# Performance work log

Measured on AMD Instinct MI355X. Metric: run time of the kernel, lower is better.

The kernel has to match this reference:

```python
import jax, jax.numpy as jnp
import numpy as np

B, S, E, H = 2, 2048, 1024, 16
D = E // H  # head_dim = 64
EPS = 1e-6


def _angle_decay():
    # angle: 1/10000**linspace(0,1,D//2), each value repeated twice (interleaved)
    a = 1.0 / (10000.0 ** jnp.linspace(0.0, 1.0, D // 2))
    angle = jnp.repeat(a, 2)  # [D]
    decay = jnp.log(1.0 - 2.0 ** (-5.0 - jnp.arange(H, dtype=jnp.float32)))  # [H]
    return angle, decay


def _rel_pos(slen):
    angle, decay = _angle_decay()
    idx = jnp.arange(slen, dtype=jnp.float32)
    sin = jnp.sin(idx[:, None] * angle[None, :])  # [S, D]
    cos = jnp.cos(idx[:, None] * angle[None, :])  # [S, D]
    diff = idx[:, None] - idx[None, :]            # [S, S]
    tril = diff >= 0
    masked = jnp.where(tril, diff, jnp.inf)
    mask = jnp.exp(masked * decay[:, None, None])  # [H, S, S]; exp(-inf)=0 on upper tri
    mask = jnp.nan_to_num(mask)
    mask = mask / jnp.sqrt(jnp.sum(mask, axis=-1, keepdims=True))
    return sin, cos, mask


def _rotate_every_two(x):
    x1 = x[..., ::2]
    x2 = x[..., 1::2]
    return jnp.stack((-x2, x1), axis=-1).reshape(x.shape)


def _theta_shift(x, sin, cos):
    # x: [B, H, S, D]; sin/cos: [S, D] broadcast over B,H
    return x * cos + _rotate_every_two(x) * sin


def setup_inputs() -> dict:
    key = jax.random.key(0)
    ks = jax.random.split(key, 5)
    scale = 1.0 / np.sqrt(E)
    return {
        "x": jax.random.normal(ks[0], (B, S, E), dtype=jnp.float32),
        "Wq": jax.random.normal(ks[1], (E, E), dtype=jnp.float32) * scale,
        "Wk": jax.random.normal(ks[2], (E, E), dtype=jnp.float32) * scale,
        "Wv": jax.random.normal(ks[3], (E, E), dtype=jnp.float32) * scale,
        "Wg": jax.random.normal(ks[4], (E, E), dtype=jnp.float32) * scale,
    }


def reference(x, Wq, Wk, Wv, Wg):
    bsz, tgt_len, _ = x.shape
    sin, cos, mask = _rel_pos(tgt_len)
    scaling = E ** (-0.5)

    q = x @ Wq
    k = (x @ Wk) * scaling
    v = x @ Wv
    g = x @ Wg

    q = q.reshape(bsz, tgt_len, H, D).transpose(0, 2, 1, 3)  # [B,H,S,D]
    k = k.reshape(bsz, tgt_len, H, D).transpose(0, 2, 1, 3)
    vr = v.reshape(bsz, tgt_len, H, D).transpose(0, 2, 1, 3)

    qr = _theta_shift(q, sin, cos)
    kr = _theta_shift(k, sin, cos)

    qk = jnp.einsum("bhqd,bhkd->bhqk", qr, kr) * mask[None]
    denom = jax.lax.stop_gradient(
        jnp.clip(jnp.sum(jnp.abs(qk), axis=-1, keepdims=True), 1.0, 5e4)
    )
    out = jnp.einsum("bhqk,bhkd->bhqd", qk / denom, vr)
    out = out.transpose(0, 2, 1, 3)  # [B,S,H,D]

    # RMSNorm over head_dim (no affine)
    out = out * jax.lax.rsqrt(jnp.mean(out * out, axis=-1, keepdims=True) + EPS)
    out = out.reshape(bsz, tgt_len, E)
    return jax.nn.silu(g) * out
```

## Files before the change

### kernel.cpp

```cpp
#include <hip/hip_runtime.h>

typedef unsigned short u16;
typedef unsigned int u32;
typedef __attribute__((ext_vector_type(8))) __bf16 bf16x8;
typedef __attribute__((ext_vector_type(4))) float f32x4;

#define B_SZ   2
#define S_LEN  2048
#define E_DIM  1024
#define NHEAD  16
#define HD     64
#define KDIM   1024
#define NQKV   3072

__device__ __forceinline__ float bf2f(u16 u){
  union { u32 i; float f; } c; c.i = ((u32)u) << 16; return c.f;
}
__device__ __forceinline__ u16 f2bf(float f){
  union { float f; u32 i; } c; c.f = f;
  return (u16)((c.i + 0x7FFFu + ((c.i >> 16) & 1u)) >> 16);
}
__device__ __forceinline__ u16 f2bf_fast(float f){
  union { float f; u32 i; } c; c.f = f;
  return (u16)((c.i + 0x8000u) >> 16);
}
__device__ __forceinline__ void gl2lds16(const void* g, void* l){
  __builtin_amdgcn_global_load_lds((const __attribute__((address_space(1))) void*)g,
                                   (__attribute__((address_space(3))) void*)l, 16, 0, 0);
}

__global__ __launch_bounds__(256) void prep_kernel(const float* __restrict__ x,
                                                   const float* __restrict__ Wq, const float* __restrict__ Wk,
                                                   const float* __restrict__ Wv, const float* __restrict__ Wg,
                                                   u16* __restrict__ xb, u16* __restrict__ WT){
  __shared__ u16 tile[64][66];
  int z = blockIdx.z;
  int t = threadIdx.x;
  if (z < 4){
    const float* Ws[4] = {Wq, Wk, Wv, Wg};
    const float* W = Ws[z];
    int n0 = blockIdx.x * 64, k0 = blockIdx.y * 64;
    int r = t >> 2, cg = (t & 3) * 16;
    const float* src = W + (size_t)(k0 + r) * E_DIM + n0 + cg;
    float f[16];
    #pragma unroll
    for (int c = 0; c < 4; c++) *(float4*)&f[c * 4] = *(const float4*)&src[c * 4];
    #pragma unroll
    for (int i = 0; i < 16; i++) tile[r][cg + i] = f2bf(f[i]);
    __syncthreads();
    u16 ov[16];
    #pragma unroll
    for (int i = 0; i < 16; i++) ov[i] = tile[cg + i][r];
    int n7 = r & 7, cb = cg >> 3;
    u16* dst = WT + (size_t)(z * E_DIM + n0 + r) * KDIM + k0;
    *(uint4*)&dst[(cb ^ n7) * 8]       = *(uint4*)&ov[0];
    *(uint4*)&dst[((cb + 1) ^ n7) * 8] = *(uint4*)&ov[8];
  } else {
    int blk = (z - 4) * 256 + blockIdx.y * 16 + blockIdx.x;
    size_t flat = ((size_t)blk * 256 + t) * 16;
    int m7 = (int)((flat >> 10) & 7);
    int cb = (int)((flat >> 3) & 7);
    size_t tl = flat & ~(size_t)63;
    float f[16];
    #pragma unroll
    for (int c = 0; c < 4; c++) *(float4*)&f[c * 4] = *(const float4*)&x[flat + c * 4];
    u16 o[16];
    #pragma unroll
    for (int i = 0; i < 16; i++) o[i] = f2bf(f[i]);
    *(uint4*)&xb[tl + ((cb ^ m7) * 8)]       = *(uint4*)&o[0];
    *(uint4*)&xb[tl + (((cb + 1) ^ m7) * 8)] = *(uint4*)&o[8];
  }
}

__global__ __launch_bounds__(512, 2) void gemm_kernel(const u16* __restrict__ A, const u16* __restrict__ Bt,
                                                      u16* __restrict__ qkv, u16* __restrict__ gc){
  __shared__ __align__(16) u16 As[2][2][128 * 64];
  __shared__ __align__(16) u16 Bs[2][2][128 * 64];
  int m0 = blockIdx.y * 256, n0 = blockIdx.x * 256;
  int t = threadIdx.x;
  int wave = t >> 6, lane = t & 63;
  int l15 = lane & 15, quad = lane >> 4, h8 = lane & 7;
  int wm = wave >> 2, wn = wave & 3;

  f32x4 acc[8][4];
  #pragma unroll
  for (int i = 0; i < 8; i++)
    #pragma unroll
    for (int j = 0; j < 4; j++) acc[i][j] = (f32x4){0.f, 0.f, 0.f, 0.f};

  auto stA = [&](int buf, int half, int kt){
    const u16* src = A + (size_t)(m0 + half * 128) * KDIM + kt * 64;
    #pragma unroll
    for (int c = 0; c < 2; c++){
      int L = c * 512 + t;
      gl2lds16(src + (size_t)(L >> 3) * KDIM + (L & 7) * 8, &As[buf][half][L * 8]);
    }
  };
  auto stB = [&](int buf, int half, int kt){
    const u16* src = Bt + (size_t)(n0 + half * 128) * KDIM + kt * 64;
    #pragma unroll
    for (int c = 0; c < 2; c++){
      int L = c * 512 + t;
      gl2lds16(src + (size_t)(L >> 3) * KDIM + (L & 7) * 8, &Bs[buf][half][L * 8]);
    }
  };
  auto ldA = [&](int buf, int i, int ks) -> bf16x8 {
    int r = i * 16 + l15;
    return *(const bf16x8*)&As[buf][wm][r * 64 + (((ks * 4 + quad) ^ h8) * 8)];
  };
  auto ldB = [&](int buf, int j, int ks) -> bf16x8 {
    int c = (wn & 1) * 64 + j * 16 + l15;
    return *(const bf16x8*)&Bs[buf][wn >> 1][c * 64 + (((ks * 4 + quad) ^ h8) * 8)];
  };

  stA(0, 0, 0); stB(0, 0, 0); stA(0, 1, 0); stB(0, 1, 0);
  asm volatile("s_waitcnt vmcnt(4)" ::: "memory");
  __builtin_amdgcn_s_barrier();

  bf16x8 a[4][2];
  bf16x8 bA[2][2];
  bf16x8 bB[2][2];

  for (int t2 = 0; t2 < 8; ++t2){
    int kt0 = 2 * t2;
    bool more = (t2 < 7);

    #pragma unroll
    for (int half = 0; half < 2; ++half){
      int buf = half;
      bool stg = (buf == 0) || more;
      {
        #pragma unroll
        for (int i = 0; i < 4; i++){ a[i][0] = ldA(buf, i, 0); a[i][1] = ldA(buf, i, 1); }
        #pragma unroll
        for (int j = 0; j < 2; j++){ bA[j][0] = ldB(buf, j, 0); bA[j][1] = ldB(buf, j, 1); }
        if (buf == 0){ stA(1, 0, kt0 + 1); stB(1, 0, kt0 + 1); }
        else if (more){ stA(0, 0, kt0 + 2); stB(0, 0, kt0 + 2); }
        __builtin_amdgcn_sched_barrier(0);
        __builtin_amdgcn_s_barrier();
        asm volatile("s_waitcnt lgkmcnt(0)" ::: "memory");
        __builtin_amdgcn_sched_barrier(0);
        __builtin_amdgcn_s_setprio(1);
        #pragma unroll
        for (int i = 0; i < 4; i++)
          #pragma unroll
          for (int j = 0; j < 2; j++){
            acc[i][j] = __builtin_amdgcn_mfma_f32_16x16x32_bf16(a[i][0], bA[j][0], acc[i][j], 0, 0, 0);
            acc[i][j] = __builtin_amdgcn_mfma_f32_16x16x32_bf16(a[i][1], bA[j][1], acc[i][j], 0, 0, 0);
          }
        __builtin_amdgcn_s_setprio(0);
        __builtin_amdgcn_sched_barrier(0);
        if (stg) { asm volatile("s_waitcnt vmcnt(4)" ::: "memory"); }
        else     { asm volatile("s_waitcnt vmcnt(0)" ::: "memory"); }
        __builtin_amdgcn_s_barrier();
      }
      {
        #pragma unroll
        for (int j = 0; j < 2; j++){ bB[j][0] = ldB(buf, j + 2, 0); bB[j][1] = ldB(buf, j + 2, 1); }
        if (buf == 0){ stA(1, 1, kt0 + 1); stB(1, 1, kt0 + 1); }
        else if (more){ stA(0, 1, kt0 + 2); stB(0, 1, kt0 + 2); }
        __builtin_amdgcn_sched_barrier(0);
        __builtin_amdgcn_s_barrier();
        asm volatile("s_waitcnt lgkmcnt(0)" ::: "memory");
        __builtin_amdgcn_sched_barrier(0);
        __builtin_amdgcn_s_setprio(1);
        #pragma unroll
        for (int i = 0; i < 4; i++)
          #pragma unroll
          for (int j = 0; j < 2; j++){
            acc[i][j + 2] = __builtin_amdgcn_mfma_f32_16x16x32_bf16(a[i][0], bB[j][0], acc[i][j + 2], 0, 0, 0);
            acc[i][j + 2] = __builtin_amdgcn_mfma_f32_16x16x32_bf16(a[i][1], bB[j][1], acc[i][j + 2], 0, 0, 0);
          }
        __builtin_amdgcn_s_setprio(0);
        __builtin_amdgcn_sched_barrier(0);
        __builtin_amdgcn_s_barrier();
      }
      {
        #pragma unroll
        for (int i = 0; i < 4; i++){ a[i][0] = ldA(buf, i + 4, 0); a[i][1] = ldA(buf, i + 4, 1); }
        __builtin_amdgcn_sched_barrier(0);
        __builtin_amdgcn_s_barrier();
        asm volatile("s_waitcnt lgkmcnt(0)" ::: "memory");
        __builtin_amdgcn_sched_barrier(0);
        __builtin_amdgcn_s_setprio(1);
        #pragma unroll
        for (int i = 0; i < 4; i++)
          #pragma unroll
          for (int j = 0; j < 2; j++){
            acc[i + 4][j + 2] = __builtin_amdgcn_mfma_f32_16x16x32_bf16(a[i][0], bB[j][0], acc[i + 4][j + 2], 0, 0, 0);
            acc[i + 4][j + 2] = __builtin_amdgcn_mfma_f32_16x16x32_bf16(a[i][1], bB[j][1], acc[i + 4][j + 2], 0, 0, 0);
          }
        #pragma unroll
        for (int i = 0; i < 4; i++)
          #pragma unroll
          for (int j = 0; j < 2; j++){
            acc[i + 4][j] = __builtin_amdgcn_mfma_f32_16x16x32_bf16(a[i][0], bA[j][0], acc[i + 4][j], 0, 0, 0);
            acc[i + 4][j] = __builtin_amdgcn_mfma_f32_16x16x32_bf16(a[i][1], bA[j][1], acc[i + 4][j], 0, 0, 0);
          }
        __builtin_amdgcn_s_setprio(0);
        __builtin_amdgcn_sched_barrier(0);
        if (stg) { asm volatile("s_waitcnt vmcnt(4)" ::: "memory"); }
        __builtin_amdgcn_s_barrier();
      }
    }
  }

  if (n0 < 3072){
    #pragma unroll
    for (int i = 0; i < 8; i++){
      int row = m0 + wm * 128 + i * 16 + quad * 4;
      #pragma unroll
      for (int j = 0; j < 4; j++){
        int col = n0 + wn * 64 + j * 16 + l15;
        #pragma unroll
        for (int r = 0; r < 4; r++)
          qkv[(size_t)(row + r) * NQKV + col] = f2bf(acc[i][j][r]);
      }
    }
  } else {
    #pragma unroll
    for (int i = 0; i < 8; i++){
      int row = m0 + wm * 128 + i * 16 + quad * 4;
      #pragma unroll
      for (int j = 0; j < 4; j++){
        int e = (n0 - 3072) + wn * 64 + j * 16 + l15;
        #pragma unroll
        for (int r = 0; r < 4; r++)
          gc[(size_t)(row + r) * E_DIM + e] = f2bf(acc[i][j][r]);
      }
    }
  }
}

__global__ __launch_bounds__(256) void shift_kernel(const u16* __restrict__ qkv,
                                                    u16* __restrict__ qr, u16* __restrict__ kr,
                                                    u16* __restrict__ vt){
  int sb = blockIdx.x, bh = blockIdx.y;
  int s0 = sb * 64;
  int t = threadIdx.x;
  int sl = t >> 2, dg = (t & 3) * 16;
  int s = s0 + sl;
  int h = bh & 15;
  size_t token = (size_t)(bh >> 4) * S_LEN + s;
  size_t base = token * NQKV + h * HD + dg;
  u16 qv[16], kv[16], vv[16];
  *(uint4*)&qv[0] = *(const uint4*)&qkv[base];
  *(uint4*)&qv[8] = *(const uint4*)&qkv[base + 8];
  *(uint4*)&kv[0] = *(const uint4*)&qkv[base + 1024];
  *(uint4*)&kv[8] = *(const uint4*)&qkv[base + 1024 + 8];
  *(uint4*)&vv[0] = *(const uint4*)&qkv[base + 2048];
  *(uint4*)&vv[8] = *(const uint4*)&qkv[base + 2048 + 8];
  u16 qo[16], ko[16];
  #pragma unroll
  for (int i = 0; i < 8; i++){
    int dd = dg + 2 * i;
    float a = exp2f(-(float)(dd >> 1) * (13.287712379549449f / 31.0f));
    float ang = (float)s * a;
    float sn, cs;
    __sincosf(ang, &sn, &cs);
    float qe = bf2f(qv[2 * i]), qd = bf2f(qv[2 * i + 1]);
    qo[2 * i]     = f2bf(qe * cs - qd * sn);
    qo[2 * i + 1] = f2bf(qd * cs + qe * sn);
    float ke = bf2f(kv[2 * i]) * 0.03125f, kd = bf2f(kv[2 * i + 1]) * 0.03125f;
    ko[2 * i]     = f2bf(ke * cs - kd * sn);
    ko[2 * i + 1] = f2bf(kd * cs + ke * sn);
  }
  size_t dsto = ((size_t)bh * S_LEN + s) * HD;
  *(uint4*)&qr[dsto + dg]     = *(uint4*)&qo[0];
  *(uint4*)&qr[dsto + dg + 8] = *(uint4*)&qo[8];
  int s7 = s & 7, cbk = dg >> 3;
  *(uint4*)&kr[dsto + ((cbk ^ s7) * 8)]       = *(uint4*)&ko[0];
  *(uint4*)&kr[dsto + (((cbk + 1) ^ s7) * 8)] = *(uint4*)&ko[8];
  __shared__ u16 vs[64][66];
  #pragma unroll
  for (int i = 0; i < 16; i++) vs[sl][dg + i] = vv[i];
  __syncthreads();
  int d = t >> 2, jg = (t & 3) * 16;
  u16 ov[16];
  #pragma unroll
  for (int i = 0; i < 16; i++) ov[i] = vs[jg + i][d];
  int d7 = d & 7, cbv = jg >> 3;
  size_t vrow = ((size_t)bh * HD + d) * S_LEN + s0;
  *(uint4*)&vt[vrow + ((cbv ^ d7) * 8)]       = *(uint4*)&ov[0];
  *(uint4*)&vt[vrow + (((cbv + 1) ^ d7) * 8)] = *(uint4*)&ov[8];
}

__global__ __launch_bounds__(256, 2) void retention_kernel(const u16* __restrict__ qr, const u16* __restrict__ kr,
                                                           const u16* __restrict__ vt,
                                                           u16* __restrict__ pO, u16* __restrict__ pBa){
  int bh = blockIdx.x;
  int qb = 15 - (int)blockIdx.y;
  int z  = blockIdx.z;
  int h = bh & 15;
  int q0 = qb * 128;
  __shared__ __align__(16) u16 Ks[2][64 * 64];
  __shared__ __align__(16) u16 Vs[2][64 * 64];
  __shared__ __align__(16) u16 Ps[128 * 72];
  int t = threadIdx.x, wave = t >> 6, lane = t & 63;
  int l15 = lane & 15, quad = lane >> 4, h8 = lane & 7;

  float decay = log1pf(-exp2f(-5.0f - (float)h));
  float negd = -decay;
  float estep = __expf(64.0f * negd);

  int qsE[2], rowb[2];
  #pragma unroll
  for (int e = 0; e < 2; e++){ rowb[e] = wave * 32 + e * 16; qsE[e] = q0 + rowb[e]; }

  bf16x8 qB[2][2];
  #pragma unroll
  for (int e = 0; e < 2; e++){
    size_t qrow = ((size_t)bh * S_LEN + qsE[e] + l15) * HD;
    qB[e][0] = *(const bf16x8*)&qr[qrow + quad * 8];
    qB[e][1] = *(const bf16x8*)&qr[qrow + 32 + quad * 8];
  }

  float win_f = 11.0f / negd;
  int win_i = (win_f > 2.1e9f) ? 0x7f000000 : (int)win_f;
  int nk = 2 * qb + 2;
  int z_lo = (z * nk) >> 2;
  int z_hi = (((z + 1) * nk) >> 2) - 1;
  int kb_lo = z_lo;
  {
    int jmin = q0 - win_i;
    if (jmin > z_lo * 64){ int wlo = jmin >> 6; kb_lo = wlo > z_lo ? wlo : z_lo; }
  }
  int k0s = kb_lo * 64;

  float em1d = expm1f(decay);
  float rfE[2]; int iE[2];
  #pragma unroll
  for (int e = 0; e < 2; e++){
    int i = qsE[e] + l15;
    iE[e] = i;
    float rowsum = expm1f((float)(i + 1) * decay) / em1d;
    rfE[e] = __expf((float)(i - k0s) * decay) * rsqrtf(rowsum);
  }
  float e1 = __expf(negd);
  float c16 = __expf(negd * 16.0f);
  float cbr[4];
  cbr[0] = __expf(negd * (float)(quad * 4));
  cbr[1] = cbr[0] * e1; cbr[2] = cbr[1] * e1; cbr[3] = cbr[2] * e1;

  f32x4 o[2][4];
  #pragma unroll
  for (int e = 0; e < 2; e++)
    #pragma unroll
    for (int dt = 0; dt < 4; dt++) o[e][dt] = (f32x4){0.f, 0.f, 0.f, 0.f};
  float babs[2] = {0.f, 0.f};

  const u16* krbh = kr + (size_t)bh * S_LEN * HD;
  const u16* vtbh = vt + (size_t)bh * HD * S_LEN;

  if (kb_lo <= z_hi){
    {
      int k0 = kb_lo * 64;
      #pragma unroll
      for (int c = 0; c < 2; c++){
        int L = c * 256 + t;
        gl2lds16(krbh + (size_t)k0 * HD + L * 8, &Ks[0][L * 8]);
      }
      #pragma unroll
      for (int c = 0; c < 2; c++){
        int L = c * 256 + t;
        gl2lds16(vtbh + (size_t)(L >> 3) * S_LEN + k0 + (L & 7) * 8, &Vs[0][L * 8]);
      }
    }
    __syncthreads();
    int cur = 0;
    for (int kb = kb_lo; kb <= z_hi; kb++){
      if (kb < z_hi){
        int k0n = (kb + 1) * 64;
        #pragma unroll
        for (int c = 0; c < 2; c++){
          int L = c * 256 + t;
          gl2lds16(krbh + (size_t)k0n * HD + L * 8, &Ks[cur ^ 1][L * 8]);
        }
        #pragma unroll
        for (int c = 0; c < 2; c++){
          int L = c * 256 + t;
          gl2lds16(vtbh + (size_t)(L >> 3) * S_LEN + k0n + (L & 7) * 8, &Vs[cur ^ 1][L * 8]);
        }
      }
      int k0 = kb * 64;
      const u16* KsC = &Ks[cur][0];
      const u16* VsC = &Vs[cur][0];

      bf16x8 kA0[4], kA1[4];
      #pragma unroll
      for (int ct = 0; ct < 4; ct++){
        int rw = (ct * 16 + l15) * 64;
        kA0[ct] = *(const bf16x8*)&KsC[rw + ((quad ^ h8) * 8)];
        kA1[ct] = *(const bf16x8*)&KsC[rw + (((quad + 4) ^ h8) * 8)];
      }
      #pragma unroll
      for (int e = 0; e < 2; e++){
        int qs = qsE[e];
        if (k0 <= qs + 15 && k0 + 63 >= qs - win_i){
          bool diag = (k0 + 64 > qs);
          float cf[4] = {cbr[0], cbr[1], cbr[2], cbr[3]};
          #pragma unroll
          for (int ct = 0; ct < 4; ct++){
            f32x4 zacc = (f32x4){0.f, 0.f, 0.f, 0.f};
            zacc = __builtin_amdgcn_mfma_f32_16x16x32_bf16(kA0[ct], qB[e][0], zacc, 0, 0, 0);
            zacc = __builtin_amdgcn_mfma_f32_16x16x32_bf16(kA1[ct], qB[e][1], zacc, 0, 0, 0);
            u16 pk[4];
            #pragma unroll
            for (int r = 0; r < 4; r++){
              float p = zacc[r] * (rfE[e] * cf[r]);
              if (diag && (k0 + ct * 16 + quad * 4 + r) > iE[e]) p = 0.f;
              babs[e] += fabsf(p);
              pk[r] = f2bf_fast(p);
              cf[r] *= c16;
            }
            u32 lo = (u32)pk[0] | ((u32)pk[1] << 16);
            u32 hi = (u32)pk[2] | ((u32)pk[3] << 16);
            *(uint2*)&Ps[(rowb[e] + l15) * 72 + ct * 16 + quad * 4] = make_uint2(lo, hi);
          }
        }
      }
      #pragma unroll
      for (int e = 0; e < 2; e++){
        int qs = qsE[e];
        if (k0 <= qs + 15 && k0 + 63 >= qs - win_i){
          bf16x8 pB0 = *(const bf16x8*)&Ps[(rowb[e] + l15) * 72 + quad * 8];
          bf16x8 pB1 = *(const bf16x8*)&Ps[(rowb[e] + l15) * 72 + 32 + quad * 8];
          #pragma unroll
          for (int dt = 0; dt < 4; dt++){
            int rw = (dt * 16 + l15) * 64;
            bf16x8 vA0 = *(const bf16x8*)&VsC[rw + ((quad ^ h8) * 8)];
            bf16x8 vA1 = *(const bf16x8*)&VsC[rw + (((quad + 4) ^ h8) * 8)];
            o[e][dt] = __builtin_amdgcn_mfma_f32_16x16x32_bf16(vA0, pB0, o[e][dt], 0, 0, 0);
            o[e][dt] = __builtin_amdgcn_mfma_f32_16x16x32_bf16(vA1, pB1, o[e][dt], 0, 0, 0);
          }
        }
      }
      #pragma unroll
      for (int e = 0; e < 2; e++) rfE[e] *= estep;
      __syncthreads();
      cur ^= 1;
    }
  }

  size_t slot = ((size_t)bh * 16 + qb) * 4 + z;
  u16* po = pO + slot * (4 * 128 * 16);
  #pragma unroll
  for (int e = 0; e < 2; e++){
    float bsum = babs[e];
    bsum += __shfl_xor(bsum, 16);
    bsum += __shfl_xor(bsum, 32);
    if (quad == 0) pBa[slot * 128 + rowb[e] + l15] = f2bf(bsum);
    #pragma unroll
    for (int dt = 0; dt < 4; dt++){
      u16 pk[4];
      #pragma unroll
      for (int r = 0; r < 4; r++) pk[r] = f2bf(o[e][dt][r]);
      *(uint2*)&po[(dt * 128 + rowb[e] + l15) * 16 + quad * 4] = *(uint2*)pk;
    }
  }
}

__global__ __launch_bounds__(128) void combine_kernel(const u16* __restrict__ pO, const u16* __restrict__ pBa,
                                                      const u16* __restrict__ gc, float* __restrict__ out){
  int bh = blockIdx.x, qb = blockIdx.y;
  int b = bh >> 4, h = bh & 15;
  int i = threadIdx.x;
  int s = qb * 128 + i;
  size_t s4 = ((size_t)bh * 16 + qb) * 4;
  float v[64];
  #pragma unroll
  for (int d = 0; d < 64; d++) v[d] = 0.f;
  float bsum = 0.f;
  #pragma unroll
  for (int z = 0; z < 4; z++){
    const u16* pz = pO + (s4 + z) * 8192;
    #pragma unroll
    for (int dt = 0; dt < 4; dt++){
      u16 a[16];
      *(uint4*)&a[0] = *(const uint4*)&pz[(dt * 128 + i) * 16];
      *(uint4*)&a[8] = *(const uint4*)&pz[(dt * 128 + i) * 16 + 8];
      #pragma unroll
      for (int c = 0; c < 16; c++) v[dt * 16 + c] += bf2f(a[c]);
    }
    bsum += bf2f(pBa[(s4 + z) * 128 + i]);
  }
  float dinv = 1.0f / fminf(fmaxf(bsum, 1.0f), 50000.0f);
  float ssq = 0.f;
  #pragma unroll
  for (int d = 0; d < 64; d++){ v[d] *= dinv; ssq += v[d] * v[d]; }
  float rms = rsqrtf(ssq * (1.0f / 64.0f) + 1e-6f);
  size_t gbase = ((size_t)b * S_LEN + s) * E_DIM + h * HD;
  u16 gu[64];
  #pragma unroll
  for (int c = 0; c < 8; c++) *(uint4*)&gu[c * 8] = *(const uint4*)&gc[gbase + c * 8];
  float ov[64];
  #pragma unroll
  for (int d = 0; d < 64; d++){
    float gv = bf2f(gu[d]);
    float sg = gv / (1.0f + __expf(-gv));
    ov[d] = v[d] * rms * sg;
  }
  float* obase = out + ((size_t)b * S_LEN + s) * E_DIM + h * HD;
  #pragma unroll
  for (int c = 0; c < 16; c++) *(float4*)&obase[c * 4] = *(float4*)&ov[c * 4];
}

extern "C" void kernel_launch(void* const* d_in, const int* in_sizes, int n_in,
                              void* d_out, int out_size, void* d_ws, size_t ws_size,
                              hipStream_t stream){
  const float* x  = (const float*)d_in[0];
  const float* Wq = (const float*)d_in[1];
  const float* Wk = (const float*)d_in[2];
  const float* Wv = (const float*)d_in[3];
  const float* Wg = (const float*)d_in[4];
  float* out = (float*)d_out;
  char* ws = (char*)d_ws;
  u16* qkv = (u16*)(ws);
  u16* pO  = (u16*)(ws);
  u16* xb  = (u16*)(ws + (32ull << 20));
  u16* qrp = (u16*)(ws + (32ull << 20));
  u16* WT  = (u16*)(ws + (40ull << 20));
  u16* krp = (u16*)(ws + (40ull << 20));
  u16* vtp = (u16*)(ws + (48ull << 20));
  u16* gcp = (u16*)(ws + (56ull << 20));
  u16* pBa = (u16*)(ws + (64ull << 20));

  prep_kernel     <<<dim3(16, 16, 8),  256, 0, stream>>>(x, Wq, Wk, Wv, Wg, xb, WT);
  gemm_kernel     <<<dim3(16, 16),     512, 0, stream>>>(xb, WT, qkv, gcp);
  shift_kernel    <<<dim3(32, 32),     256, 0, stream>>>(qkv, qrp, krp, vtp);
  retention_kernel<<<dim3(32, 16, 4),  256, 0, stream>>>(qrp, krp, vtp, pO, pBa);
  combine_kernel  <<<dim3(32, 16),     128, 0, stream>>>(pO, pBa, gcp, out);
}
```

Before: 185.5 us.

## Fuse rotary shift and V transpose into GEMM epilogue, drop shift kernel

Removes the separate shift kernel. The QKV GEMM epilogue now applies the rotary theta shift and K scaling, using a lane shuffle to get the paired element, and writes Q, swizzled K and transposed, swizzled V directly in the layouts the retention kernel reads. This avoids writing and re-reading the bf16 qkv intermediate and saves one launch. In exchange the epilogue does scattered 2-byte stores for Q/K plus sincos work inside the GEMM, and the workspace layout is reshuffled so xb and WT no longer overlap the Q/K buffers.

New measurement: 191.2 us. 1.03x slower.

```diff
diff --git a/kernel.cpp b/kernel.cpp
--- a/kernel.cpp
+++ b/kernel.cpp
@@ -11,7 +11,6 @@
 #define NHEAD  16
 #define HD     64
 #define KDIM   1024
-#define NQKV   3072
 
 __device__ __forceinline__ float bf2f(u16 u){
   union { u32 i; float f; } c; c.i = ((u32)u) << 16; return c.f;
@@ -73,7 +72,8 @@
 }
 
 __global__ __launch_bounds__(512, 2) void gemm_kernel(const u16* __restrict__ A, const u16* __restrict__ Bt,
-                                                      u16* __restrict__ qkv, u16* __restrict__ gc){
+                                                      u16* __restrict__ qr, u16* __restrict__ kr,
+                                                      u16* __restrict__ vt, u16* __restrict__ gc){
   __shared__ __align__(16) u16 As[2][2][128 * 64];
   __shared__ __align__(16) u16 Bs[2][2][128 * 64];
   int m0 = blockIdx.y * 256, n0 = blockIdx.x * 256;
@@ -205,84 +205,70 @@
     }
   }
 
-  if (n0 < 3072){
+  int zone = n0 >> 10;
+  int n0l = n0 & 1023;
+  int hh = (n0l >> 6) + wn;
+
+  if (zone == 3){
     #pragma unroll
     for (int i = 0; i < 8; i++){
       int row = m0 + wm * 128 + i * 16 + quad * 4;
       #pragma unroll
       for (int j = 0; j < 4; j++){
-        int col = n0 + wn * 64 + j * 16 + l15;
-        #pragma unroll
-        for (int r = 0; r < 4; r++)
-          qkv[(size_t)(row + r) * NQKV + col] = f2bf(acc[i][j][r]);
-      }
-    }
-  } else {
-    #pragma unroll
-    for (int i = 0; i < 8; i++){
-      int row = m0 + wm * 128 + i * 16 + quad * 4;
-      #pragma unroll
-      for (int j = 0; j < 4; j++){
-        int e = (n0 - 3072) + wn * 64 + j * 16 + l15;
+        int e = n0l + wn * 64 + j * 16 + l15;
         #pragma unroll
         for (int r = 0; r < 4; r++)
           gc[(size_t)(row + r) * E_DIM + e] = f2bf(acc[i][j][r]);
       }
     }
-  }
-}
-
-__global__ __launch_bounds__(256) void shift_kernel(const u16* __restrict__ qkv,
-                                                    u16* __restrict__ qr, u16* __restrict__ kr,
-                                                    u16* __restrict__ vt){
-  int sb = blockIdx.x, bh = blockIdx.y;
-  int s0 = sb * 64;
-  int t = threadIdx.x;
-  int sl = t >> 2, dg = (t & 3) * 16;
-  int s = s0 + sl;
-  int h = bh & 15;
-  size_t token = (size_t)(bh >> 4) * S_LEN + s;
-  size_t base = token * NQKV + h * HD + dg;
-  u16 qv[16], kv[16], vv[16];
-  *(uint4*)&qv[0] = *(const uint4*)&qkv[base];
-  *(uint4*)&qv[8] = *(const uint4*)&qkv[base + 8];
-  *(uint4*)&kv[0] = *(const uint4*)&qkv[base + 1024];
-  *(uint4*)&kv[8] = *(const uint4*)&qkv[base + 1024 + 8];
-  *(uint4*)&vv[0] = *(const uint4*)&qkv[base + 2048];
-  *(uint4*)&vv[8] = *(const uint4*)&qkv[base + 2048 + 8];
-  u16 qo[16], ko[16];
-  #pragma unroll
-  for (int i = 0; i < 8; i++){
-    int dd = dg + 2 * i;
-    float a = exp2f(-(float)(dd >> 1) * (13.287712379549449f / 31.0f));
-    float ang = (float)s * a;
-    float sn, cs;
-    __sincosf(ang, &sn, &cs);
-    float qe = bf2f(qv[2 * i]), qd = bf2f(qv[2 * i + 1]);
-    qo[2 * i]     = f2bf(qe * cs - qd * sn);
-    qo[2 * i + 1] = f2bf(qd * cs + qe * sn);
-    float ke = bf2f(kv[2 * i]) * 0.03125f, kd = bf2f(kv[2 * i + 1]) * 0.03125f;
-    ko[2 * i]     = f2bf(ke * cs - kd * sn);
-    ko[2 * i + 1] = f2bf(kd * cs + ke * sn);
-  }
-  size_t dsto = ((size_t)bh * S_LEN + s) * HD;
-  *(uint4*)&qr[dsto + dg]     = *(uint4*)&qo[0];
-  *(uint4*)&qr[dsto + dg + 8] = *(uint4*)&qo[8];
-  int s7 = s & 7, cbk = dg >> 3;
-  *(uint4*)&kr[dsto + ((cbk ^ s7) * 8)]       = *(uint4*)&ko[0];
-  *(uint4*)&kr[dsto + (((cbk + 1) ^ s7) * 8)] = *(uint4*)&ko[8];
-  __shared__ u16 vs[64][66];
-  #pragma unroll
-  for (int i = 0; i < 16; i++) vs[sl][dg + i] = vv[i];
-  __syncthreads();
-  int d = t >> 2, jg = (t & 3) * 16;
-  u16 ov[16];
-  #pragma unroll
-  for (int i = 0; i < 16; i++) ov[i] = vs[jg + i][d];
-  int d7 = d & 7, cbv = jg >> 3;
-  size_t vrow = ((size_t)bh * HD + d) * S_LEN + s0;
-  *(uint4*)&vt[vrow + ((cbv ^ d7) * 8)]       = *(uint4*)&ov[0];
-  *(uint4*)&vt[vrow + (((cbv + 1) ^ d7) * 8)] = *(uint4*)&ov[8];
+  } else if (zone == 2){
+    #pragma unroll
+    for (int i = 0; i < 8; i++){
+      int srow = m0 + wm * 128 + i * 16 + quad * 4;
+      int b = srow >> 11, sb = srow & 2047;
+      #pragma unroll
+      for (int j = 0; j < 4; j++){
+        int d = j * 16 + l15;
+        size_t rowb = ((size_t)((b << 4) + hh) * HD + d) * S_LEN;
+        u16 pk[4];
+        #pragma unroll
+        for (int r = 0; r < 4; r++) pk[r] = f2bf(acc[i][j][r]);
+        u32 lo = (u32)pk[0] | ((u32)pk[1] << 16);
+        u32 hi = (u32)pk[2] | ((u32)pk[3] << 16);
+        size_t off = rowb + (size_t)(sb & ~63) + (size_t)(((((sb >> 3) & 7) ^ (d & 7)) << 3) + (sb & 7));
+        *(uint2*)&vt[off] = make_uint2(lo, hi);
+      }
+    }
+  } else {
+    float scale = (zone == 1) ? 0.03125f : 1.0f;
+    float sgn = (l15 & 1) ? 1.0f : -1.0f;
+    #pragma unroll
+    for (int j = 0; j < 4; j++){
+      int d = j * 16 + l15;
+      float af = exp2f(-(float)(d >> 1) * (13.287712379549449f / 31.0f));
+      #pragma unroll
+      for (int i = 0; i < 8; i++){
+        int srow = m0 + wm * 128 + i * 16 + quad * 4;
+        int b = srow >> 11, sbase = srow & 2047;
+        size_t base = (size_t)((b << 4) + hh) * S_LEN;
+        #pragma unroll
+        for (int r = 0; r < 4; r++){
+          int s = sbase + r;
+          float vv = acc[i][j][r] * scale;
+          float p = __shfl_xor(vv, 1);
+          float sn, cs;
+          __sincosf((float)s * af, &sn, &cs);
+          float outv = vv * cs + sgn * p * sn;
+          u16 ob = f2bf(outv);
+          if (zone == 0){
+            qr[(base + s) * HD + d] = ob;
+          } else {
+            kr[(base + s) * HD + (((((d >> 3) & 7) ^ (s & 7)) << 3) + (d & 7))] = ob;
+          }
+        }
+      }
+    }
+  }
 }
 
 __global__ __launch_bounds__(256, 2) void retention_kernel(const u16* __restrict__ qr, const u16* __restrict__ kr,
@@ -515,19 +501,17 @@
   const float* Wg = (const float*)d_in[4];
   float* out = (float*)d_out;
   char* ws = (char*)d_ws;
-  u16* qkv = (u16*)(ws);
+  u16* xb  = (u16*)(ws);
+  u16* WT  = (u16*)(ws + (8ull  << 20));
   u16* pO  = (u16*)(ws);
-  u16* xb  = (u16*)(ws + (32ull << 20));
   u16* qrp = (u16*)(ws + (32ull << 20));
-  u16* WT  = (u16*)(ws + (40ull << 20));
   u16* krp = (u16*)(ws + (40ull << 20));
   u16* vtp = (u16*)(ws + (48ull << 20));
   u16* gcp = (u16*)(ws + (56ull << 20));
   u16* pBa = (u16*)(ws + (64ull << 20));
 
   prep_kernel     <<<dim3(16, 16, 8),  256, 0, stream>>>(x, Wq, Wk, Wv, Wg, xb, WT);
-  gemm_kernel     <<<dim3(16, 16),     512, 0, stream>>>(xb, WT, qkv, gcp);
-  shift_kernel    <<<dim3(32, 32),     256, 0, stream>>>(qkv, qrp, krp, vtp);
+  gemm_kernel     <<<dim3(16, 16),     512, 0, stream>>>(xb, WT, qrp, krp, vtp, gcp);
   retention_kernel<<<dim3(32, 16, 4),  256, 0, stream>>>(qrp, krp, vtp, pO, pBa);
   combine_kernel  <<<dim3(32, 16),     128, 0, stream>>>(pO, pBa, gcp, out);
 }
```
